# Kernel optimization log

Hardware: AMD Instinct MI355X
Metric: run time of the kernel (lower is better)

The kernel has to match this reference:

```python
import jax, jax.numpy as jnp
import numpy as np

PRUNE_N, PRUNE_M = 2, 4
RIA_A = 1.0
NUM_HEADS = 16
HEAD_DIM = 128
ROPE_THETA = 10000.0


def sparse_mask(W, scaler_row, perm):
    # RIA metric: |W|/colsum + |W|/rowsum, scaled by sqrt(scaler_row)**a
    absW = jnp.abs(W)
    metric = (absW / absW.sum(axis=0, keepdims=True)
              + absW / absW.sum(axis=1, keepdims=True))
    metric = metric * (jnp.sqrt(scaler_row)[None, :] ** RIA_A)
    Wm = metric @ perm                      # permute columns: [R, C]
    R, C = Wm.shape
    nb = C // PRUNE_M
    blocks = Wm.reshape(R, nb, PRUNE_M)
    # hard N:M mask: top-n per block of m
    _, idx = jax.lax.top_k(blocks, PRUNE_N)           # [R, nb, n]
    hard = jax.nn.one_hot(idx, PRUNE_M, dtype=Wm.dtype).sum(axis=-2)  # [R, nb, m]
    soft = jax.nn.softmax(blocks, axis=-1)
    hard = hard.reshape(R, C) @ perm.T
    soft = soft.reshape(R, C) @ perm.T
    # straight-through estimator
    return jax.lax.stop_gradient(hard - soft) + soft


def sparse_linear(x, W, b, scaler_row, perm):
    Wm = W * sparse_mask(W, scaler_row, perm)
    y = jnp.einsum('bsh,oh->bso', x, Wm)
    return y + b if b is not None else y


def rotate_half(x):
    x1, x2 = jnp.split(x, 2, axis=-1)
    return jnp.concatenate([-x2, x1], axis=-1)


def rope_tables(seq_len, dim, dtype):
    inv_freq = 1.0 / (ROPE_THETA ** (jnp.arange(0, dim, 2, dtype=jnp.float32) / dim))
    t = jnp.arange(seq_len, dtype=jnp.float32)
    freqs = jnp.outer(t, inv_freq)               # [S, dim/2]
    emb = jnp.concatenate([freqs, freqs], axis=-1)  # [S, dim]
    return jnp.cos(emb).astype(dtype), jnp.sin(emb).astype(dtype)


def setup_inputs() -> dict:
    key = jax.random.key(0)
    ks = jax.random.split(key, 16)
    H = 2048
    B, S = 2, 2048
    inp = {
        'hidden_states': jax.random.normal(ks[0], (B, S, H), jnp.float32) * 0.02,
        'Wq': jax.random.normal(ks[1], (H, H), jnp.float32) * 0.02,
        'bq': jax.random.normal(ks[2], (H,), jnp.float32) * 0.02,
        'Wk': jax.random.normal(ks[3], (H, H), jnp.float32) * 0.02,
        'bk': jax.random.normal(ks[4], (H,), jnp.float32) * 0.02,
        'Wv': jax.random.normal(ks[5], (H, H), jnp.float32) * 0.02,
        'bv': jax.random.normal(ks[6], (H,), jnp.float32) * 0.02,
        'Wo': jax.random.normal(ks[7], (H, H), jnp.float32) * 0.02,
        'sq': jax.random.uniform(ks[8], (H,), jnp.float32, 0.1, 1.0),
        'sk': jax.random.uniform(ks[9], (H,), jnp.float32, 0.1, 1.0),
        'sv': jax.random.uniform(ks[10], (H,), jnp.float32, 0.1, 1.0),
        'so': jax.random.uniform(ks[11], (H,), jnp.float32, 0.1, 1.0),
        'perm_qkv': jax.random.normal(ks[12], (H, H), jnp.float32) * 0.02,
        'perm_o': jax.random.normal(ks[13], (H, H), jnp.float32) * 0.02,
        'position_ids': jnp.broadcast_to(jnp.arange(S, dtype=jnp.int64), (B, S)),
    }
    return inp


def reference(hidden_states, Wq, bq, Wk, bk, Wv, bv, Wo,
              sq, sk, sv, so, perm_qkv, perm_o, position_ids):
    B, S, H = hidden_states.shape
    q = sparse_linear(hidden_states, Wq, bq, sq, perm_qkv)
    k = sparse_linear(hidden_states, Wk, bk, sk, perm_qkv)
    v = sparse_linear(hidden_states, Wv, bv, sv, perm_qkv)

    q = q.reshape(B, S, NUM_HEADS, HEAD_DIM).transpose(0, 2, 1, 3)  # [B,Hh,S,D]
    k = k.reshape(B, S, NUM_HEADS, HEAD_DIM).transpose(0, 2, 1, 3)
    v = v.reshape(B, S, NUM_HEADS, HEAD_DIM).transpose(0, 2, 1, 3)

    cos, sin = rope_tables(S, HEAD_DIM, q.dtype)
    c = cos[position_ids][:, None]  # [B,1,S,D]
    s = sin[position_ids][:, None]
    q = q * c + rotate_half(q) * s
    k = k * c + rotate_half(k) * s

    scores = jnp.einsum('bhqd,bhkd->bhqk', q, k) / np.sqrt(HEAD_DIM)
    causal = jnp.tril(jnp.ones((S, S), dtype=bool))
    scores = jnp.where(causal[None, None], scores, jnp.finfo(jnp.float32).min)
    attn = jax.nn.softmax(scores.astype(jnp.float32), axis=-1).astype(q.dtype)
    out = jnp.einsum('bhqk,bhkd->bhqd', attn, v)
    out = out.transpose(0, 2, 1, 3).reshape(B, S, H)
    out = sparse_linear(out, Wo, None, so, perm_o)
    return out
```

## Files before the change

kernel.cpp:

```cpp
#include <hip/hip_runtime.h>
#include <cstdint>
#include <cstddef>

typedef __attribute__((ext_vector_type(4))) float  f32x4;
typedef __attribute__((ext_vector_type(4))) int    i32x4;
typedef __attribute__((ext_vector_type(8))) short  s16x8;
typedef __attribute__((ext_vector_type(4))) short  s16x4;
typedef __attribute__((ext_vector_type(8))) __bf16 bf16x8;

struct Ptr4 { const float* p[4]; };

#define DEV __device__ __forceinline__

DEV unsigned short f2bf_u(float x) {
  unsigned u = __builtin_bit_cast(unsigned, x);
  u += 0x7fffu + ((u >> 16) & 1u);
  return (unsigned short)(u >> 16);
}
DEV float bfu2f(unsigned short u) {
  return __builtin_bit_cast(float, ((unsigned)u) << 16);
}
DEV bf16x8 ld_frag(const unsigned short* p) {
  s16x8 v = *(const s16x8*)p;
  return __builtin_bit_cast(bf16x8, v);
}
DEV f32x4 mfma16(bf16x8 a, bf16x8 b, f32x4 c) {
  return __builtin_amdgcn_mfma_f32_16x16x32_bf16(a, b, c, 0, 0, 0);
}
DEV void gload_lds16(const unsigned short* g, unsigned short* l) {
  __builtin_amdgcn_global_load_lds(
      (const __attribute__((address_space(1))) unsigned int*)g,
      (__attribute__((address_space(3))) unsigned int*)l, 16, 0, 0);
}

__global__ __launch_bounds__(256)
void k_rowsum(Ptr4 Ws, float* __restrict__ rowsums)
{
  const int row = blockIdx.x, mat = blockIdx.y, tid = threadIdx.x;
  const float* W = Ws.p[mat] + (size_t)row * 2048;
  float s = 0.f;
  #pragma unroll
  for (int p = 0; p < 2; ++p) {
    f32x4 v = *(const f32x4*)(W + p * 1024 + tid * 4);
    s += fabsf(v[0]) + fabsf(v[1]) + fabsf(v[2]) + fabsf(v[3]);
  }
  #pragma unroll
  for (int off = 1; off < 64; off <<= 1) s += __shfl_xor(s, off);
  __shared__ float red[4];
  if ((tid & 63) == 0) red[tid >> 6] = s;
  __syncthreads();
  if (tid == 0) rowsums[mat * 2048 + row] = red[0] + red[1] + red[2] + red[3];
}

__global__ __launch_bounds__(256)
void k_colsum_part(Ptr4 Ws, float* __restrict__ part)
{
  const int c = blockIdx.x * 256 + threadIdx.x;
  const int r0 = blockIdx.y * 64;
  const int mat = blockIdx.z;
  const float* W = Ws.p[mat];
  float s = 0.f;
  for (int rr = 0; rr < 64; ++rr) s += fabsf(W[(size_t)(r0 + rr) * 2048 + c]);
  part[((size_t)mat * 32 + blockIdx.y) * 2048 + c] = s;
}
__global__ __launch_bounds__(256)
void k_colsum_red(const float* __restrict__ part, float* __restrict__ colsums)
{
  const int gid = blockIdx.x * 256 + threadIdx.x;
  const int mat = gid >> 11, c = gid & 2047;
  float s = 0.f;
  #pragma unroll
  for (int j = 0; j < 32; ++j) s += part[((size_t)mat * 32 + j) * 2048 + c];
  colsums[gid] = s;
}

__global__ __launch_bounds__(256)
void k_metric(Ptr4 Ws, Ptr4 Ss, const float* __restrict__ rowsums,
              const float* __restrict__ colsums,
              unsigned short* __restrict__ mhi, unsigned short* __restrict__ mlo)
{
  const size_t idx4 = ((size_t)blockIdx.x * 256 + threadIdx.x) * 4;
  const int row = (int)(idx4 >> 11);
  const int c = (int)(idx4 & 2047);
  const int mat = row >> 11, rl = row & 2047;
  const float rs = rowsums[mat * 2048 + rl];
  f32x4 w  = *(const f32x4*)(Ws.p[mat] + (size_t)rl * 2048 + c);
  f32x4 cs = *(const f32x4*)(colsums + mat * 2048 + c);
  f32x4 sv = *(const f32x4*)(Ss.p[mat] + c);
  s16x4 hv, lv;
  #pragma unroll
  for (int j = 0; j < 4; ++j) {
    const float a = fabsf(w[j]);
    const float m = (a / cs[j] + a / rs) * sqrtf(sv[j]);
    const unsigned short hb = f2bf_u(m);
    hv[j] = (short)hb;
    lv[j] = (short)f2bf_u(m - bfu2f(hb));
  }
  *(s16x4*)(mhi + idx4) = hv;
  *(s16x4*)(mlo + idx4) = lv;
}

__global__ __launch_bounds__(256)
void k_perm_prep(const float* __restrict__ pq, const float* __restrict__ po,
                 unsigned short* __restrict__ thi_q, unsigned short* __restrict__ tlo_q,
                 unsigned short* __restrict__ thi_o, unsigned short* __restrict__ tlo_o,
                 unsigned short* __restrict__ pb_q, unsigned short* __restrict__ pb_o)
{
  __shared__ float T[64 * 65];
  const int which = blockIdx.z;
  const float* src = which ? po : pq;
  unsigned short* thi = which ? thi_o : thi_q;
  unsigned short* tlo = which ? tlo_o : tlo_q;
  unsigned short* pb  = which ? pb_o : pb_q;
  const int rb = blockIdx.y * 64, cb = blockIdx.x * 64, tid = threadIdx.x;
  #pragma unroll
  for (int i = 0; i < 4; ++i) {
    const int cc = i * 256 + tid;
    const int rowl = cc >> 4, c4 = (cc & 15) * 4;
    f32x4 v = *(const f32x4*)(src + (size_t)(rb + rowl) * 2048 + cb + c4);
    s16x4 pc;
    #pragma unroll
    for (int j = 0; j < 4; ++j) {
      T[rowl * 65 + c4 + j] = v[j];
      pc[j] = (short)f2bf_u(v[j]);
    }
    *(s16x4*)(pb + (size_t)(rb + rowl) * 2048 + cb + c4) = pc;
  }
  __syncthreads();
  #pragma unroll
  for (int i = 0; i < 4; ++i) {
    const int cc = i * 256 + tid;
    const int rowt = cc >> 4, c4 = (cc & 15) * 4;
    s16x4 hh, ll;
    #pragma unroll
    for (int j = 0; j < 4; ++j) {
      const float v = T[(c4 + j) * 65 + rowt];
      const unsigned short hb = f2bf_u(v);
      hh[j] = (short)hb;
      ll[j] = (short)f2bf_u(v - bfu2f(hb));
    }
    const size_t off = (size_t)(cb + rowt) * 2048 + rb + c4;
    *(s16x4*)(thi + off) = hh;
    *(s16x4*)(tlo + off) = ll;
  }
}

__global__ __launch_bounds__(256)
void k_cast_bf(const float* __restrict__ src, unsigned short* __restrict__ dst)
{
  const size_t i = ((size_t)blockIdx.x * 256 + threadIdx.x) * 8;
  f32x4 a = *(const f32x4*)(src + i);
  f32x4 b = *(const f32x4*)(src + i + 4);
  s16x8 o;
  #pragma unroll
  for (int j = 0; j < 4; ++j) o[j] = (short)f2bf_u(a[j]);
  #pragma unroll
  for (int j = 0; j < 4; ++j) o[4 + j] = (short)f2bf_u(b[j]);
  *(s16x8*)(dst + i) = o;
}

__global__ __launch_bounds__(256)
void k_rope_tab(float* __restrict__ ct, float* __restrict__ st)
{
  const int gid = blockIdx.x * 256 + threadIdx.x;
  const int s = gid >> 6, i = gid & 63;
  const float ex = (float)(2 * i) / 128.f;
  const float inv = 1.f / powf(10000.f, ex);
  const float f = (float)s * inv;
  ct[gid] = cosf(f);
  st[gid] = sinf(f);
}

__global__ __launch_bounds__(256)
void k_rope_reshape(const unsigned short* __restrict__ yqkv, const int* __restrict__ pos,
                    const float* __restrict__ ct, const float* __restrict__ st,
                    unsigned short* __restrict__ qo, unsigned short* __restrict__ ko)
{
  const int gid = blockIdx.x * 256 + threadIdx.x;
  const int d = gid & 127;
  const int s = (gid >> 7) & 2047;
  const int h = (gid >> 18) & 15;
  const int b = gid >> 22;
  const int t = b * 2048 + s;
  const int p = pos[t];
  const int dh = d & 63;
  const float cv = ct[p * 64 + dh], svv = st[p * 64 + dh];
  const size_t yb = (size_t)t * 6144 + h * 128;
  const float q0 = bfu2f(yqkv[yb + d]);
  const float k0 = bfu2f(yqkv[yb + 2048 + d]);
  const int pd = (d < 64) ? d + 64 : d - 64;
  float q1 = bfu2f(yqkv[yb + pd]);
  float k1 = bfu2f(yqkv[yb + 2048 + pd]);
  if (d < 64) { q1 = -q1; k1 = -k1; }
  const size_t o = ((size_t)(b * 16 + h) * 2048 + s) * 128 + d;
  qo[o] = f2bf_u(q0 * cv + q1 * svv);
  ko[o] = f2bf_u(k0 * cv + k1 * svv);
}

__global__ __launch_bounds__(256)
void k_vtrans(const unsigned short* __restrict__ yqkv, unsigned short* __restrict__ vt)
{
  __shared__ float T[64 * 129];
  const int st = blockIdx.x, bh = blockIdx.y, tid = threadIdx.x;
  const int b = bh >> 4, h = bh & 15;
  #pragma unroll
  for (int i = 0; i < 4; ++i) {
    const int c = i * 256 + tid;
    const int sl = c >> 4, d8 = (c & 15) * 8;
    s16x8 v = *(const s16x8*)(yqkv + (size_t)(b * 2048 + st * 64 + sl) * 6144 + 4096 + h * 128 + d8);
    #pragma unroll
    for (int j = 0; j < 8; ++j) T[sl * 129 + d8 + j] = bfu2f((unsigned short)v[j]);
  }
  __syncthreads();
  #pragma unroll
  for (int i = 0; i < 4; ++i) {
    const int c = i * 256 + tid;
    const int d = c >> 3, s8 = (c & 7) * 8;
    s16x8 o;
    #pragma unroll
    for (int j = 0; j < 8; ++j) o[j] = (short)f2bf_u(T[(s8 + j) * 129 + d]);
    *(s16x8*)(vt + ((size_t)bh * 128 + d) * 2048 + st * 64 + s8) = o;
  }
}

template<int MODE, int SPLIT>
__global__ __launch_bounds__(256)
void gemm_bt(const unsigned short* __restrict__ Ahi, const unsigned short* __restrict__ Alo,
             const unsigned short* __restrict__ Bhi_1, const unsigned short* __restrict__ Blo_1,
             const unsigned short* __restrict__ Bhi_2, const unsigned short* __restrict__ Blo_2,
             int bswitch,
             float* __restrict__ Cf, unsigned short* __restrict__ Cb,
             Ptr4 aux, int M, int N, int K)
{
  __shared__ alignas(16) unsigned short As[2 * 4096];
  __shared__ alignas(16) unsigned short Bs[2 * 4096];
  const int tid = threadIdx.x;
  const int lane = tid & 63, wid = tid >> 6;
  const int wm = wid >> 1, wn = wid & 1;
  const int r = lane & 15, g = lane >> 4;
  const int mbase = blockIdx.y * 128;
  const int nbase = blockIdx.x * 128;
  const int KT = K >> 5;
  (void)M;
  const unsigned short* Bhi = (mbase >= bswitch) ? Bhi_2 : Bhi_1;
  const unsigned short* Blo = (mbase >= bswitch) ? Blo_2 : Blo_1;

  const f32x4 zero = {0.f, 0.f, 0.f, 0.f};
  f32x4 acc[4][4];
  #pragma unroll
  for (int i = 0; i < 4; ++i) {
    #pragma unroll
    for (int j = 0; j < 4; ++j) acc[i][j] = zero;
  }

  const int srl = lane >> 2;
  const int sch = lane & 3;

  auto issue_tile = [&](int kt, int buf) {
    const size_t kb = (size_t)kt * 32;
    #pragma unroll
    for (int i = 0; i < 2; ++i) {
      const int rbase = wid * 32 + i * 16;
      const int rloc = rbase + srl;
      const int sc = ((sch ^ ((rloc >> 1) & 3)) << 3);
      const size_t ga = (size_t)(mbase + rloc) * K + kb + sc;
      const size_t gb = (size_t)(nbase + rloc) * K + kb + sc;
      gload_lds16(Ahi + ga, &As[buf * 4096 + rbase * 32]);
      gload_lds16(Bhi + gb, &Bs[buf * 4096 + rbase * 32]);
      if (SPLIT) {
        gload_lds16(Alo + ga, &As[4096 + rbase * 32]);
        gload_lds16(Blo + gb, &Bs[4096 + rbase * 32]);
      }
    }
  };

  if (SPLIT) {
    issue_tile(0, 0);
    for (int kt = 0; kt < KT; ++kt) {
      __syncthreads();

      bf16x8 ah[4], bfr[4], al[4], bl[4];
      #pragma unroll
      for (int mi = 0; mi < 4; ++mi) {
        const int arow = wm * 64 + mi * 16 + r;
        const int sw = ((g ^ ((arow >> 1) & 3)) << 3);
        ah[mi] = ld_frag(&As[arow * 32 + sw]);
        al[mi] = ld_frag(&As[4096 + arow * 32 + sw]);
      }
      #pragma unroll
      for (int ni = 0; ni < 4; ++ni) {
        const int brow = wn * 64 + ni * 16 + r;
        const int sw = ((g ^ ((brow >> 1) & 3)) << 3);
        bfr[ni] = ld_frag(&Bs[brow * 32 + sw]);
        bl[ni] = ld_frag(&Bs[4096 + brow * 32 + sw]);
      }
      __syncthreads();
      if (kt + 1 < KT) issue_tile(kt + 1, 0);

      #pragma unroll
      for (int mi = 0; mi < 4; ++mi) {
        #pragma unroll
        for (int ni = 0; ni < 4; ++ni) {
          acc[mi][ni] = mfma16(al[mi], bfr[ni], acc[mi][ni]);
          acc[mi][ni] = mfma16(ah[mi], bl[ni], acc[mi][ni]);
          acc[mi][ni] = mfma16(ah[mi], bfr[ni], acc[mi][ni]);
        }
      }
    }
  } else {
    issue_tile(0, 0);
    int cur = 0;
    for (int kt = 0; kt < KT; ++kt) {
      __syncthreads();
      if (kt + 1 < KT) issue_tile(kt + 1, cur ^ 1);

      bf16x8 ah[4], bfr[4];
      #pragma unroll
      for (int mi = 0; mi < 4; ++mi) {
        const int arow = wm * 64 + mi * 16 + r;
        ah[mi] = ld_frag(&As[cur * 4096 + arow * 32 + ((g ^ ((arow >> 1) & 3)) << 3)]);
      }
      #pragma unroll
      for (int ni = 0; ni < 4; ++ni) {
        const int brow = wn * 64 + ni * 16 + r;
        bfr[ni] = ld_frag(&Bs[cur * 4096 + brow * 32 + ((g ^ ((brow >> 1) & 3)) << 3)]);
      }
      #pragma unroll
      for (int mi = 0; mi < 4; ++mi) {
        #pragma unroll
        for (int ni = 0; ni < 4; ++ni)
          acc[mi][ni] = mfma16(ah[mi], bfr[ni], acc[mi][ni]);
      }
      cur ^= 1;
    }
  }

  #pragma unroll
  for (int mi = 0; mi < 4; ++mi) {
    #pragma unroll
    for (int ni = 0; ni < 4; ++ni) {
      const int row0 = mbase + wm * 64 + mi * 16 + g * 4;
      const int col  = nbase + wn * 64 + ni * 16 + r;
      if (MODE == 0) {
        #pragma unroll
        for (int e = 0; e < 4; ++e)
          Cf[(size_t)(row0 + e) * N + col] = acc[mi][ni][e];
      } else if (MODE == 1) {
        const float* wsrc = aux.p[row0 >> 11];
        #pragma unroll
        for (int e = 0; e < 4; ++e) {
          const float mval = wsrc[(size_t)((row0 + e) & 2047) * 2048 + col];
          Cb[(size_t)(row0 + e) * N + col] = f2bf_u(acc[mi][ni][e] * mval);
        }
      } else if (MODE == 2) {
        const float* bp = aux.p[col >> 11];
        const float bb = bp[col & 2047];
        #pragma unroll
        for (int e = 0; e < 4; ++e)
          Cb[(size_t)(row0 + e) * N + col] = f2bf_u(acc[mi][ni][e] + bb);
      } else {
        const int ii = r & 3;
        #pragma unroll
        for (int e = 0; e < 4; ++e) {
          const float v  = acc[mi][ni][e];
          const float v1 = __shfl_xor(v, 1);
          const float v2 = __shfl_xor(v, 2);
          const float v3 = __shfl_xor(v, 3);
          int cnt = 0;
          { const int j = ii ^ 1; cnt += (v1 > v) || (v1 == v && j < ii); }
          { const int j = ii ^ 2; cnt += (v2 > v) || (v2 == v && j < ii); }
          { const int j = ii ^ 3; cnt += (v3 > v) || (v3 == v && j < ii); }
          Cb[(size_t)(row0 + e) * N + col] =
              (cnt < 2) ? (unsigned short)0x3F80 : (unsigned short)0;
        }
      }
    }
  }
}

__global__ __launch_bounds__(256)
void attn_fa(const unsigned short* __restrict__ Qh, const unsigned short* __restrict__ Kh,
             const unsigned short* __restrict__ Vt, unsigned short* __restrict__ Out)
{
  __shared__ alignas(16) unsigned short Ks[64 * 128];
  __shared__ alignas(16) unsigned short Vs[128 * 64];
  __shared__ alignas(16) unsigned short Ps[4][1024];
  const int tid = threadIdx.x, lane = tid & 63, wid = tid >> 6;
  const int r = lane & 15, g = lane >> 4;
  const int pair = blockIdx.x, bh = blockIdx.y;
  const int b = bh >> 4, h = bh & 15;
  const f32x4 zero = {0.f, 0.f, 0.f, 0.f};

  i32x4 kr[4], vr[4];
  auto issue_kv = [&](int kvt) {
    #pragma unroll
    for (int i = 0; i < 4; ++i) {
      const int c = i * 256 + tid;
      {
        const int row = c >> 4, slot = c & 15;
        kr[i] = *(const i32x4*)(Kh + ((size_t)bh * 2048 + kvt * 64 + row) * 128 + slot * 8);
      }
      {
        const int row = c >> 3, slot = c & 7;
        vr[i] = *(const i32x4*)(Vt + ((size_t)bh * 128 + row) * 2048 + kvt * 64 + slot * 8);
      }
    }
  };

  for (int half = 0; half < 2; ++half) {
    const int qt = half ? (31 - pair) : pair;
    const int qrow0 = qt * 64 + wid * 16;

    bf16x8 qf[4];
    {
      const unsigned short* qp = Qh + ((size_t)bh * 2048 + qrow0 + r) * 128;
      #pragma unroll
      for (int ks = 0; ks < 4; ++ks) qf[ks] = ld_frag(qp + ks * 32 + g * 8);
    }
    f32x4 oacc[8];
    #pragma unroll
    for (int i = 0; i < 8; ++i) oacc[i] = zero;
    float m_run[4] = {-1e30f, -1e30f, -1e30f, -1e30f};
    float l_run[4] = {0.f, 0.f, 0.f, 0.f};

    issue_kv(0);
    for (int kvt = 0; kvt <= qt; ++kvt) {
      __syncthreads();
      #pragma unroll
      for (int i = 0; i < 4; ++i) {
        const int c = i * 256 + tid;
        {
          const int row = c >> 4, slot = c & 15;
          *(i32x4*)&Ks[row * 128 + ((slot ^ (row & 7)) << 3)] = kr[i];
        }
        {
          const int row = c >> 3, slot = c & 7;
          *(i32x4*)&Vs[row * 64 + ((slot ^ (row & 7)) << 3)] = vr[i];
        }
      }
      __syncthreads();
      if (kvt < qt) issue_kv(kvt + 1);

      f32x4 sc[4];
      #pragma unroll
      for (int ni = 0; ni < 4; ++ni) sc[ni] = zero;
      #pragma unroll
      for (int ks = 0; ks < 4; ++ks) {
        const int slot = (ks << 2) | g;
        #pragma unroll
        for (int ni = 0; ni < 4; ++ni) {
          const int krow = ni * 16 + r;
          bf16x8 kf = ld_frag(&Ks[krow * 128 + ((slot ^ (krow & 7)) << 3)]);
          sc[ni] = mfma16(qf[ks], kf, sc[ni]);
        }
      }
      const float sscale = 0.08838834764831845f;
      if (kvt == qt) {
        #pragma unroll
        for (int ni = 0; ni < 4; ++ni) {
          const int kvg = kvt * 64 + ni * 16 + r;
          #pragma unroll
          for (int e = 0; e < 4; ++e) {
            const int qg = qrow0 + g * 4 + e;
            const float s = sc[ni][e] * sscale;
            sc[ni][e] = (kvg > qg) ? -1e30f : s;
          }
        }
      } else {
        #pragma unroll
        for (int ni = 0; ni < 4; ++ni) {
          #pragma unroll
          for (int e = 0; e < 4; ++e) sc[ni][e] *= sscale;
        }
      }
      float corr[4];
      #pragma unroll
      for (int e = 0; e < 4; ++e) {
        float mx = fmaxf(fmaxf(sc[0][e], sc[1][e]), fmaxf(sc[2][e], sc[3][e]));
        mx = fmaxf(mx, __shfl_xor(mx, 1));
        mx = fmaxf(mx, __shfl_xor(mx, 2));
        mx = fmaxf(mx, __shfl_xor(mx, 4));
        mx = fmaxf(mx, __shfl_xor(mx, 8));
        const float mn = fmaxf(m_run[e], mx);
        corr[e] = exp2f((m_run[e] - mn) * 1.4426950408889634f);
        m_run[e] = mn;
      }
      float psum[4] = {0.f, 0.f, 0.f, 0.f};
      #pragma unroll
      for (int ni = 0; ni < 4; ++ni) {
        #pragma unroll
        for (int e = 0; e < 4; ++e) {
          const float p = exp2f((sc[ni][e] - m_run[e]) * 1.4426950408889634f);
          sc[ni][e] = p;
          psum[e] += p;
        }
      }
      #pragma unroll
      for (int e = 0; e < 4; ++e) {
        float s = psum[e];
        s += __shfl_xor(s, 1);
        s += __shfl_xor(s, 2);
        s += __shfl_xor(s, 4);
        s += __shfl_xor(s, 8);
        l_run[e] = l_run[e] * corr[e] + s;
      }
      #pragma unroll
      for (int nf = 0; nf < 8; ++nf) {
        #pragma unroll
        for (int e = 0; e < 4; ++e) oacc[nf][e] *= corr[e];
      }
      #pragma unroll
      for (int ni = 0; ni < 4; ++ni) {
        #pragma unroll
        for (int e = 0; e < 4; ++e) {
          const int prow = g * 4 + e;
          const int col = ni * 16 + r;
          const int slot = col >> 3;
          Ps[wid][prow * 64 + ((slot ^ (prow & 7)) << 3) + (col & 7)] = f2bf_u(sc[ni][e]);
        }
      }
      #pragma unroll
      for (int ks = 0; ks < 2; ++ks) {
        const int slot = (ks << 2) | g;
        bf16x8 pf = ld_frag(&Ps[wid][r * 64 + ((slot ^ (r & 7)) << 3)]);
        #pragma unroll
        for (int nf = 0; nf < 8; ++nf) {
          const int vrow = nf * 16 + r;
          bf16x8 vf = ld_frag(&Vs[vrow * 64 + ((slot ^ (vrow & 7)) << 3)]);
          oacc[nf] = mfma16(pf, vf, oacc[nf]);
        }
      }
    }
    #pragma unroll
    for (int e = 0; e < 4; ++e) {
      const float inv = 1.f / l_run[e];
      const int qg = qrow0 + g * 4 + e;
      #pragma unroll
      for (int nf = 0; nf < 8; ++nf) {
        const int d = nf * 16 + r;
        Out[((size_t)(b * 2048 + qg)) * 2048 + h * 128 + d] = f2bf_u(oacc[nf][e] * inv);
      }
    }
  }
}

extern "C" void kernel_launch(void* const* d_in, const int* in_sizes, int n_in,
                              void* d_out, int out_size, void* d_ws, size_t ws_size,
                              hipStream_t stream)
{
  (void)in_sizes; (void)n_in; (void)out_size; (void)ws_size;
  const float* hid   = (const float*)d_in[0];
  const float* Wq    = (const float*)d_in[1];
  const float* bq    = (const float*)d_in[2];
  const float* Wk    = (const float*)d_in[3];
  const float* bk    = (const float*)d_in[4];
  const float* Wv    = (const float*)d_in[5];
  const float* bv    = (const float*)d_in[6];
  const float* Wo    = (const float*)d_in[7];
  const float* sq    = (const float*)d_in[8];
  const float* sk    = (const float*)d_in[9];
  const float* sv    = (const float*)d_in[10];
  const float* so    = (const float*)d_in[11];
  const float* permq = (const float*)d_in[12];
  const float* permo = (const float*)d_in[13];
  const int* pos     = (const int*)d_in[14];
  float* out = (float*)d_out;
  char* ws = (char*)d_ws;

  constexpr size_t OFF_ROWS = 0;
  constexpr size_t OFF_COLS = OFF_ROWS + (size_t)4 * 2048 * 4;
  constexpr size_t OFF_PART = OFF_COLS + (size_t)4 * 2048 * 4;
  constexpr size_t OFF_COS  = OFF_PART + (size_t)4 * 32 * 2048 * 4;
  constexpr size_t OFF_SIN  = OFF_COS + (size_t)2048 * 64 * 4;
  constexpr size_t SZ_PERM  = (size_t)2048 * 2048 * 2;
  constexpr size_t OFF_A    = OFF_SIN + (size_t)2048 * 64 * 4;
  constexpr size_t OFF_PTQH = OFF_A;
  constexpr size_t OFF_PTQL = OFF_PTQH + SZ_PERM;
  constexpr size_t OFF_PTOH = OFF_PTQL + SZ_PERM;
  constexpr size_t OFF_PTOL = OFF_PTOH + SZ_PERM;
  constexpr size_t OFF_PBQ  = OFF_PTOL + SZ_PERM;
  constexpr size_t OFF_PBO  = OFF_PBQ + SZ_PERM;
  constexpr size_t SZ_M8    = (size_t)8192 * 2048 * 2;
  constexpr size_t OFF_B    = OFF_PBO + SZ_PERM;
  constexpr size_t OFF_C    = OFF_B + SZ_M8;
  constexpr size_t OFF_D    = OFF_C + SZ_M8;
  constexpr size_t OFF_E    = OFF_D + SZ_M8;

  float* rowsums = (float*)(ws + OFF_ROWS);
  float* colsums = (float*)(ws + OFF_COLS);
  float* part    = (float*)(ws + OFF_PART);
  float* cost    = (float*)(ws + OFF_COS);
  float* sint    = (float*)(ws + OFF_SIN);
  unsigned short* ptqh = (unsigned short*)(ws + OFF_PTQH);
  unsigned short* ptql = (unsigned short*)(ws + OFF_PTQL);
  unsigned short* ptoh = (unsigned short*)(ws + OFF_PTOH);
  unsigned short* ptol = (unsigned short*)(ws + OFF_PTOL);
  unsigned short* pbq  = (unsigned short*)(ws + OFF_PBQ);
  unsigned short* pbo  = (unsigned short*)(ws + OFF_PBO);
  unsigned short* mhi  = (unsigned short*)(ws + OFF_B);
  unsigned short* mlo  = (unsigned short*)(ws + OFF_C);
  unsigned short* hard = (unsigned short*)(ws + OFF_D);
  unsigned short* wfin = (unsigned short*)(ws + OFF_E);
  unsigned short* yqkv = (unsigned short*)(ws + OFF_B);
  unsigned short* qhb  = (unsigned short*)(ws + OFF_A);
  unsigned short* khb  = (unsigned short*)(ws + OFF_A + 2 * SZ_PERM);
  unsigned short* vtg  = (unsigned short*)(ws + OFF_A + 4 * SZ_PERM);
  unsigned short* xbf  = (unsigned short*)(ws + OFF_D);
  unsigned short* att  = (unsigned short*)(ws + OFF_D + SZ_M8 / 2);

  Ptr4 Wptrs{{Wq, Wk, Wv, Wo}};
  Ptr4 Sptrs{{sq, sk, sv, so}};
  Ptr4 BiasP{{bq, bk, bv, nullptr}};
  Ptr4 NoAux{{nullptr, nullptr, nullptr, nullptr}};
  constexpr int NOSW = 1 << 30;

  k_rowsum<<<dim3(2048, 4), 256, 0, stream>>>(Wptrs, rowsums);
  k_colsum_part<<<dim3(8, 32, 4), 256, 0, stream>>>(Wptrs, part);
  k_colsum_red<<<32, 256, 0, stream>>>(part, colsums);
  k_metric<<<16384, 256, 0, stream>>>(Wptrs, Sptrs, rowsums, colsums, mhi, mlo);
  k_perm_prep<<<dim3(32, 32, 2), 256, 0, stream>>>(permq, permo, ptqh, ptql, ptoh, ptol, pbq, pbo);
  gemm_bt<3, 1><<<dim3(16, 64), 256, 0, stream>>>(mhi, mlo, ptqh, ptql, ptoh, ptol, 6144,
                                                  nullptr, hard, NoAux, 8192, 2048, 2048);
  gemm_bt<1, 0><<<dim3(16, 64), 256, 0, stream>>>(hard, nullptr, pbq, nullptr, pbo, nullptr, 6144,
                                                  nullptr, wfin, Wptrs, 8192, 2048, 2048);
  k_cast_bf<<<4096, 256, 0, stream>>>(hid, xbf);
  gemm_bt<2, 0><<<dim3(48, 32), 256, 0, stream>>>(xbf, nullptr, wfin, nullptr, wfin, nullptr, NOSW,
                                                  nullptr, yqkv, BiasP, 4096, 6144, 2048);
  k_rope_tab<<<512, 256, 0, stream>>>(cost, sint);
  k_rope_reshape<<<32768, 256, 0, stream>>>(yqkv, pos, cost, sint, qhb, khb);
  k_vtrans<<<dim3(32, 32), 256, 0, stream>>>(yqkv, vtg);
  attn_fa<<<dim3(16, 32), 256, 0, stream>>>(qhb, khb, vtg, att);
  gemm_bt<0, 0><<<dim3(16, 32), 256, 0, stream>>>(att, nullptr, wfin + (size_t)6144 * 2048, nullptr,
                                                  wfin + (size_t)6144 * 2048, nullptr, NOSW,
                                                  out, nullptr, NoAux, 4096, 2048, 2048);
}
```

Before: 663.2 us.

## Use 256-row GEMM tiles and XCD-aware block swizzle for GEMMs and attention

Adds a BIG template option to the GEMM that grows the M tile from 128 to 256 rows, so each B tile loaded into shared memory is reused across twice as many rows and the grid is halved for the mask, weight-finalisation and QKV GEMMs. It also remaps block IDs so that consecutive logical tiles land on the same XCD, aiming at better L2 locality, and applies the same remap to the attention kernel. The larger tile doubles the accumulator registers and A-tile LDS, which risks lower occupancy or spills. Halving the grid may also leave some of the device's compute units underused.

```diff
diff --git a/kernel.cpp b/kernel.cpp
--- a/kernel.cpp
+++ b/kernel.cpp
@@ -31,6 +31,10 @@
   __builtin_amdgcn_global_load_lds(
       (const __attribute__((address_space(1))) unsigned int*)g,
       (__attribute__((address_space(3))) unsigned int*)l, 16, 0, 0);
+}
+DEV int xcd_swizzle(int bid, int nwg) {
+  const int q8 = nwg >> 3;
+  return (bid & 7) * q8 + (bid >> 3);
 }
 
 __global__ __launch_bounds__(256)
@@ -223,7 +227,7 @@
   }
 }
 
-template<int MODE, int SPLIT>
+template<int MODE, int SPLIT, int BIG>
 __global__ __launch_bounds__(256)
 void gemm_bt(const unsigned short* __restrict__ Ahi, const unsigned short* __restrict__ Alo,
              const unsigned short* __restrict__ Bhi_1, const unsigned short* __restrict__ Blo_1,
@@ -232,23 +236,29 @@
              float* __restrict__ Cf, unsigned short* __restrict__ Cb,
              Ptr4 aux, int M, int N, int K)
 {
-  __shared__ alignas(16) unsigned short As[2 * 4096];
+  constexpr int BM  = BIG ? 256 : 128;
+  constexpr int MI  = BM / 32;
+  constexpr int AST = BM * 32;
+  __shared__ alignas(16) unsigned short As[2 * AST];
   __shared__ alignas(16) unsigned short Bs[2 * 4096];
   const int tid = threadIdx.x;
   const int lane = tid & 63, wid = tid >> 6;
   const int wm = wid >> 1, wn = wid & 1;
   const int r = lane & 15, g = lane >> 4;
-  const int mbase = blockIdx.y * 128;
-  const int nbase = blockIdx.x * 128;
+  const int nwg = gridDim.x * gridDim.y;
+  const int sw = xcd_swizzle(blockIdx.y * gridDim.x + blockIdx.x, nwg);
+  const int tx = sw % gridDim.x, ty = sw / gridDim.x;
+  const int mbase = ty * BM;
+  const int nbase = tx * 128;
   const int KT = K >> 5;
   (void)M;
   const unsigned short* Bhi = (mbase >= bswitch) ? Bhi_2 : Bhi_1;
   const unsigned short* Blo = (mbase >= bswitch) ? Blo_2 : Blo_1;
 
   const f32x4 zero = {0.f, 0.f, 0.f, 0.f};
-  f32x4 acc[4][4];
-  #pragma unroll
-  for (int i = 0; i < 4; ++i) {
+  f32x4 acc[MI][4];
+  #pragma unroll
+  for (int i = 0; i < MI; ++i) {
     #pragma unroll
     for (int j = 0; j < 4; ++j) acc[i][j] = zero;
   }
@@ -258,19 +268,23 @@
 
   auto issue_tile = [&](int kt, int buf) {
     const size_t kb = (size_t)kt * 32;
+    #pragma unroll
+    for (int i = 0; i < BM / 64; ++i) {
+      const int rbase = wid * (BM / 4) + i * 16;
+      const int rloc = rbase + srl;
+      const int sc = ((sch ^ ((rloc >> 1) & 3)) << 3);
+      const size_t ga = (size_t)(mbase + rloc) * K + kb + sc;
+      gload_lds16(Ahi + ga, &As[buf * AST + rbase * 32]);
+      if (SPLIT) gload_lds16(Alo + ga, &As[AST + rbase * 32]);
+    }
     #pragma unroll
     for (int i = 0; i < 2; ++i) {
       const int rbase = wid * 32 + i * 16;
       const int rloc = rbase + srl;
       const int sc = ((sch ^ ((rloc >> 1) & 3)) << 3);
-      const size_t ga = (size_t)(mbase + rloc) * K + kb + sc;
       const size_t gb = (size_t)(nbase + rloc) * K + kb + sc;
-      gload_lds16(Ahi + ga, &As[buf * 4096 + rbase * 32]);
       gload_lds16(Bhi + gb, &Bs[buf * 4096 + rbase * 32]);
-      if (SPLIT) {
-        gload_lds16(Alo + ga, &As[4096 + rbase * 32]);
-        gload_lds16(Blo + gb, &Bs[4096 + rbase * 32]);
-      }
+      if (SPLIT) gload_lds16(Blo + gb, &Bs[4096 + rbase * 32]);
     }
   };
 
@@ -279,26 +293,26 @@
     for (int kt = 0; kt < KT; ++kt) {
       __syncthreads();
 
-      bf16x8 ah[4], bfr[4], al[4], bl[4];
-      #pragma unroll
-      for (int mi = 0; mi < 4; ++mi) {
-        const int arow = wm * 64 + mi * 16 + r;
-        const int sw = ((g ^ ((arow >> 1) & 3)) << 3);
-        ah[mi] = ld_frag(&As[arow * 32 + sw]);
-        al[mi] = ld_frag(&As[4096 + arow * 32 + sw]);
+      bf16x8 ah[MI], al[MI], bfr[4], bl[4];
+      #pragma unroll
+      for (int mi = 0; mi < MI; ++mi) {
+        const int arow = wm * (BM / 2) + mi * 16 + r;
+        const int sw2 = ((g ^ ((arow >> 1) & 3)) << 3);
+        ah[mi] = ld_frag(&As[arow * 32 + sw2]);
+        al[mi] = ld_frag(&As[AST + arow * 32 + sw2]);
       }
       #pragma unroll
       for (int ni = 0; ni < 4; ++ni) {
         const int brow = wn * 64 + ni * 16 + r;
-        const int sw = ((g ^ ((brow >> 1) & 3)) << 3);
-        bfr[ni] = ld_frag(&Bs[brow * 32 + sw]);
-        bl[ni] = ld_frag(&Bs[4096 + brow * 32 + sw]);
+        const int sw2 = ((g ^ ((brow >> 1) & 3)) << 3);
+        bfr[ni] = ld_frag(&Bs[brow * 32 + sw2]);
+        bl[ni] = ld_frag(&Bs[4096 + brow * 32 + sw2]);
       }
       __syncthreads();
       if (kt + 1 < KT) issue_tile(kt + 1, 0);
 
       #pragma unroll
-      for (int mi = 0; mi < 4; ++mi) {
+      for (int mi = 0; mi < MI; ++mi) {
         #pragma unroll
         for (int ni = 0; ni < 4; ++ni) {
           acc[mi][ni] = mfma16(al[mi], bfr[ni], acc[mi][ni]);
@@ -314,11 +328,11 @@
       __syncthreads();
       if (kt + 1 < KT) issue_tile(kt + 1, cur ^ 1);
 
-      bf16x8 ah[4], bfr[4];
-      #pragma unroll
-      for (int mi = 0; mi < 4; ++mi) {
-        const int arow = wm * 64 + mi * 16 + r;
-        ah[mi] = ld_frag(&As[cur * 4096 + arow * 32 + ((g ^ ((arow >> 1) & 3)) << 3)]);
+      bf16x8 ah[MI], bfr[4];
+      #pragma unroll
+      for (int mi = 0; mi < MI; ++mi) {
+        const int arow = wm * (BM / 2) + mi * 16 + r;
+        ah[mi] = ld_frag(&As[cur * AST + arow * 32 + ((g ^ ((arow >> 1) & 3)) << 3)]);
       }
       #pragma unroll
       for (int ni = 0; ni < 4; ++ni) {
@@ -326,7 +340,7 @@
         bfr[ni] = ld_frag(&Bs[cur * 4096 + brow * 32 + ((g ^ ((brow >> 1) & 3)) << 3)]);
       }
       #pragma unroll
-      for (int mi = 0; mi < 4; ++mi) {
+      for (int mi = 0; mi < MI; ++mi) {
         #pragma unroll
         for (int ni = 0; ni < 4; ++ni)
           acc[mi][ni] = mfma16(ah[mi], bfr[ni], acc[mi][ni]);
@@ -336,10 +350,10 @@
   }
 
   #pragma unroll
-  for (int mi = 0; mi < 4; ++mi) {
+  for (int mi = 0; mi < MI; ++mi) {
     #pragma unroll
     for (int ni = 0; ni < 4; ++ni) {
-      const int row0 = mbase + wm * 64 + mi * 16 + g * 4;
+      const int row0 = mbase + wm * (BM / 2) + mi * 16 + g * 4;
       const int col  = nbase + wn * 64 + ni * 16 + r;
       if (MODE == 0) {
         #pragma unroll
@@ -387,7 +401,8 @@
   __shared__ alignas(16) unsigned short Ps[4][1024];
   const int tid = threadIdx.x, lane = tid & 63, wid = tid >> 6;
   const int r = lane & 15, g = lane >> 4;
-  const int pair = blockIdx.x, bh = blockIdx.y;
+  const int sw = xcd_swizzle(blockIdx.y * gridDim.x + blockIdx.x, gridDim.x * gridDim.y);
+  const int pair = sw % 16, bh = sw / 16;
   const int b = bh >> 4, h = bh & 15;
   const f32x4 zero = {0.f, 0.f, 0.f, 0.f};
 
@@ -619,18 +634,18 @@
   k_colsum_red<<<32, 256, 0, stream>>>(part, colsums);
   k_metric<<<16384, 256, 0, stream>>>(Wptrs, Sptrs, rowsums, colsums, mhi, mlo);
   k_perm_prep<<<dim3(32, 32, 2), 256, 0, stream>>>(permq, permo, ptqh, ptql, ptoh, ptol, pbq, pbo);
-  gemm_bt<3, 1><<<dim3(16, 64), 256, 0, stream>>>(mhi, mlo, ptqh, ptql, ptoh, ptol, 6144,
-                                                  nullptr, hard, NoAux, 8192, 2048, 2048);
-  gemm_bt<1, 0><<<dim3(16, 64), 256, 0, stream>>>(hard, nullptr, pbq, nullptr, pbo, nullptr, 6144,
-                                                  nullptr, wfin, Wptrs, 8192, 2048, 2048);
+  gemm_bt<3, 1, 1><<<dim3(16, 32), 256, 0, stream>>>(mhi, mlo, ptqh, ptql, ptoh, ptol, 6144,
+                                                     nullptr, hard, NoAux, 8192, 2048, 2048);
+  gemm_bt<1, 0, 1><<<dim3(16, 32), 256, 0, stream>>>(hard, nullptr, pbq, nullptr, pbo, nullptr, 6144,
+                                                     nullptr, wfin, Wptrs, 8192, 2048, 2048);
   k_cast_bf<<<4096, 256, 0, stream>>>(hid, xbf);
-  gemm_bt<2, 0><<<dim3(48, 32), 256, 0, stream>>>(xbf, nullptr, wfin, nullptr, wfin, nullptr, NOSW,
-                                                  nullptr, yqkv, BiasP, 4096, 6144, 2048);
+  gemm_bt<2, 0, 1><<<dim3(48, 16), 256, 0, stream>>>(xbf, nullptr, wfin, nullptr, wfin, nullptr, NOSW,
+                                                     nullptr, yqkv, BiasP, 4096, 6144, 2048);
   k_rope_tab<<<512, 256, 0, stream>>>(cost, sint);
   k_rope_reshape<<<32768, 256, 0, stream>>>(yqkv, pos, cost, sint, qhb, khb);
   k_vtrans<<<dim3(32, 32), 256, 0, stream>>>(yqkv, vtg);
   attn_fa<<<dim3(16, 32), 256, 0, stream>>>(qhb, khb, vtg, att);
-  gemm_bt<0, 0><<<dim3(16, 32), 256, 0, stream>>>(att, nullptr, wfin + (size_t)6144 * 2048, nullptr,
-                                                  wfin + (size_t)6144 * 2048, nullptr, NOSW,
-                                                  out, nullptr, NoAux, 4096, 2048, 2048);
-}
+  gemm_bt<0, 0, 0><<<dim3(16, 32), 256, 0, stream>>>(att, nullptr, wfin + (size_t)6144 * 2048, nullptr,
+                                                     wfin + (size_t)6144 * 2048, nullptr, NOSW,
+                                                     out, nullptr, NoAux, 4096, 2048, 2048);
+}
```

Result: slower. 785.5 us (+18.4%).
